# Kernel tuning notes

Measured on AMD Instinct MI355X. Metric: run time of the kernel, lower is better.

The kernel has to match this reference:

```python
import jax, jax.numpy as jnp
import numpy as np

B, D = 65536, 1024

def setup_inputs() -> dict:
    key = jax.random.key(0)
    x = jax.random.normal(key, (B, D), dtype=jnp.float32)
    return {"x": x}

def reference(x) -> jnp.ndarray:
    d = x.shape[1]
    # suffix_norm[:, i] = ||x[:, i:]|| via reverse cumulative sum of squares (single O(D) pass)
    suffix_norm = jnp.sqrt(jnp.cumsum((x * x)[:, ::-1], axis=1)[:, ::-1])
    r = suffix_norm[:, :1]                                   # [B, 1] full norm
    phi = jnp.arccos(x[:, : d - 1] / suffix_norm[:, : d - 1])  # [B, D-1]
    # last angle gets sign correction from the final coordinate
    phi_last = jnp.where(x[:, -1] < 0, 2.0 * jnp.pi - phi[:, -1], phi[:, -1])
    return jnp.concatenate([r, phi[:, : d - 2], phi_last[:, None]], axis=1)
```

## Files before the change

### kernel.cpp

```cpp
#include <hip/hip_runtime.h>
#include <math.h>


#define D_DIM 1024
#define TPB 256

typedef float v4f __attribute__((ext_vector_type(4)));

template <int CTRL>
__device__ __forceinline__ float dpp0(float x) {
    return __builtin_bit_cast(
        float, __builtin_amdgcn_update_dpp(0, __builtin_bit_cast(int, x),
                                           CTRL, 0xF, 0xF, true));
}

__device__ __forceinline__ float rdlane(float x, int l) {
    return __builtin_bit_cast(
        float, __builtin_amdgcn_readlane(__builtin_bit_cast(int, x), l));
}

__device__ __forceinline__ float fast_acos(float x) {
    float a = fabsf(x);
    float p = fmaf(a, -0.0012624911f, 0.0066700901f);
    p = fmaf(p, a, -0.0170881256f);
    p = fmaf(p, a, 0.0308918810f);
    p = fmaf(p, a, -0.0501743046f);
    p = fmaf(p, a, 0.0889789874f);
    p = fmaf(p, a, -0.2145988016f);
    p = fmaf(p, a, 1.5707963050f);
    float r = sqrtf(1.0f - a) * p;
    return x < 0.0f ? 3.14159274101257f - r : r;
}

__device__ __forceinline__ float ang(float num, float den) {
    float r = num * rsqrtf(den);
    r = fminf(1.0f, fmaxf(-1.0f, r));
    return fast_acos(r);
}

__global__ __launch_bounds__(TPB) void tohypersphere_kernel(
    const float* __restrict__ x, float* __restrict__ out) {
    const int t = threadIdx.x;
    const int lane = t & 63;
    const int wave = t >> 6;
    const int r16 = lane >> 4;
    const size_t row_off = (size_t)blockIdx.x * D_DIM;

    const float4 v = ((const float4*)(x + row_off))[t];

    const float s3 = v.w * v.w;
    const float s2 = fmaf(v.z, v.z, s3);
    const float s1 = fmaf(v.y, v.y, s2);
    const float s0 = fmaf(v.x, v.x, s1);

    float ts = s0;
    ts += dpp0<0x101>(ts);
    ts += dpp0<0x102>(ts);
    ts += dpp0<0x104>(ts);
    ts += dpp0<0x108>(ts);

    const float R0 = rdlane(ts, 0);
    const float R1 = rdlane(ts, 16);
    const float R2 = rdlane(ts, 32);
    const float R3 = rdlane(ts, 48);

    float after_rows = 0.0f;
    if (r16 < 1) after_rows += R1;
    if (r16 < 2) after_rows += R2;
    if (r16 < 3) after_rows += R3;
    const float incl_wave = ts + after_rows;
    const float wtot = (R0 + R1) + (R2 + R3);

    __shared__ float wave_tot[4];
    __shared__ float edge_xw[4];
    if (lane == 0) wave_tot[wave] = wtot;
    if (lane == 63) edge_xw[wave] = v.w;

    float xw_prev = __shfl_up(v.w, 1, 64);

    __syncthreads();

    float after_waves = 0.0f;
#pragma unroll
    for (int w = 1; w < 4; ++w)
        if (w > wave) after_waves += wave_tot[w];
    if (lane == 0 && wave > 0) xw_prev = edge_xw[wave - 1];

    const float incl = incl_wave + after_waves;
    const float excl = incl - s0;

    float o0, o1, o2, o3;
    o1 = ang(v.x, incl);
    o2 = ang(v.y, s1 + excl);
    o3 = ang(v.z, s2 + excl);
    if (t == 0) {
        o0 = sqrtf(incl);
    } else {
        o0 = ang(xw_prev, fmaf(xw_prev, xw_prev, incl));
    }
    if (t == TPB - 1 && v.w < 0.0f) {
        o3 = 6.283185307179586476f - o3;
    }

    v4f tv = {o0, o1, o2, o3};
    ((v4f*)(out + row_off))[t] = tv;
}

extern "C" void kernel_launch(void* const* d_in, const int* in_sizes, int n_in,
                              void* d_out, int out_size, void* d_ws, size_t ws_size,
                              hipStream_t stream) {
    const float* x = (const float*)d_in[0];
    float* out = (float*)d_out;
    const int B = in_sizes[0] / D_DIM;
    tohypersphere_kernel<<<B, TPB, 0, stream>>>(x, out);
}
```

Before: 411.9 us.

## Use persistent grid-stride blocks with next-row prefetch and double-buffered scratch

Replaces one-block-per-row launch with a fixed grid of persistent blocks that loop over rows with a grid stride. The next row is loaded before the current row is processed, and the shared-memory scratch is double-buffered so a single barrier per row suffices. This aims to cut block launch overhead and hide load latency, at the cost of fewer independent blocks to supply memory-level parallelism.

```diff
diff --git a/kernel.cpp b/kernel.cpp
--- a/kernel.cpp
+++ b/kernel.cpp
@@ -4,6 +4,7 @@
 
 #define D_DIM 1024
 #define TPB 256
+#define NBLK 2048
 
 typedef float v4f __attribute__((ext_vector_type(4)));
 
@@ -39,71 +40,94 @@
 }
 
 __global__ __launch_bounds__(TPB) void tohypersphere_kernel(
-    const float* __restrict__ x, float* __restrict__ out) {
+    const float* __restrict__ x, float* __restrict__ out, int n_rows) {
     const int t = threadIdx.x;
     const int lane = t & 63;
     const int wave = t >> 6;
     const int r16 = lane >> 4;
-    const size_t row_off = (size_t)blockIdx.x * D_DIM;
 
-    const float4 v = ((const float4*)(x + row_off))[t];
+    __shared__ float wave_tot[2][4];
+    __shared__ float edge_xw[2][4];
 
-    const float s3 = v.w * v.w;
-    const float s2 = fmaf(v.z, v.z, s3);
-    const float s1 = fmaf(v.y, v.y, s2);
-    const float s0 = fmaf(v.x, v.x, s1);
+    const int stride = gridDim.x;
+    int row = blockIdx.x;
+    if (row >= n_rows) return;
 
-    float ts = s0;
-    ts += dpp0<0x101>(ts);
-    ts += dpp0<0x102>(ts);
-    ts += dpp0<0x104>(ts);
-    ts += dpp0<0x108>(ts);
+    const float4* __restrict__ xp = (const float4*)x + t;
+    v4f* __restrict__ op = (v4f*)out + t;
 
-    const float R0 = rdlane(ts, 0);
-    const float R1 = rdlane(ts, 16);
-    const float R2 = rdlane(ts, 32);
-    const float R3 = rdlane(ts, 48);
+    float4 vc = xp[(size_t)row * (D_DIM / 4)];
 
-    float after_rows = 0.0f;
-    if (r16 < 1) after_rows += R1;
-    if (r16 < 2) after_rows += R2;
-    if (r16 < 3) after_rows += R3;
-    const float incl_wave = ts + after_rows;
-    const float wtot = (R0 + R1) + (R2 + R3);
+    int p = 0;
+    while (true) {
+        const int nrow = row + stride;
+        const bool more = (nrow < n_rows);
+        float4 vn;
+        if (more) vn = xp[(size_t)nrow * (D_DIM / 4)];
 
-    __shared__ float wave_tot[4];
-    __shared__ float edge_xw[4];
-    if (lane == 0) wave_tot[wave] = wtot;
-    if (lane == 63) edge_xw[wave] = v.w;
+        const float4 v = vc;
+        const float s3v = v.w * v.w;
+        const float s2v = fmaf(v.z, v.z, s3v);
+        const float s1v = fmaf(v.y, v.y, s2v);
+        const float s0v = fmaf(v.x, v.x, s1v);
 
-    float xw_prev = __shfl_up(v.w, 1, 64);
+        float ts = s0v;
+        ts += dpp0<0x101>(ts);
+        ts += dpp0<0x102>(ts);
+        ts += dpp0<0x104>(ts);
+        ts += dpp0<0x108>(ts);
 
-    __syncthreads();
+        const float R0 = rdlane(ts, 0);
+        const float R1 = rdlane(ts, 16);
+        const float R2 = rdlane(ts, 32);
+        const float R3 = rdlane(ts, 48);
 
-    float after_waves = 0.0f;
+        float after_rows = 0.0f;
+        if (r16 < 1) after_rows += R1;
+        if (r16 < 2) after_rows += R2;
+        if (r16 < 3) after_rows += R3;
+        const float incl_wave = ts + after_rows;
+        const float wtot = (R0 + R1) + (R2 + R3);
+
+        if (lane == 0) wave_tot[p][wave] = wtot;
+        if (lane == 63) edge_xw[p][wave] = v.w;
+
+        float xw_prev = __shfl_up(v.w, 1, 64);
+
+        asm volatile("s_waitcnt lgkmcnt(0)" ::: "memory");
+        __builtin_amdgcn_s_barrier();
+        __builtin_amdgcn_sched_barrier(0);
+
+        float after_waves = 0.0f;
 #pragma unroll
-    for (int w = 1; w < 4; ++w)
-        if (w > wave) after_waves += wave_tot[w];
-    if (lane == 0 && wave > 0) xw_prev = edge_xw[wave - 1];
+        for (int w = 1; w < 4; ++w)
+            if (w > wave) after_waves += wave_tot[p][w];
+        if (lane == 0 && wave > 0) xw_prev = edge_xw[p][wave - 1];
 
-    const float incl = incl_wave + after_waves;
-    const float excl = incl - s0;
+        const float incl = incl_wave + after_waves;
+        const float excl = incl - s0v;
 
-    float o0, o1, o2, o3;
-    o1 = ang(v.x, incl);
-    o2 = ang(v.y, s1 + excl);
-    o3 = ang(v.z, s2 + excl);
-    if (t == 0) {
-        o0 = sqrtf(incl);
-    } else {
-        o0 = ang(xw_prev, fmaf(xw_prev, xw_prev, incl));
+        float o0, o1, o2, o3;
+        o1 = ang(v.x, incl);
+        o2 = ang(v.y, s1v + excl);
+        o3 = ang(v.z, s2v + excl);
+        if (t == 0) {
+            o0 = sqrtf(incl);
+        } else {
+            o0 = ang(xw_prev, fmaf(xw_prev, xw_prev, incl));
+        }
+        if (t == TPB - 1 && v.w < 0.0f) {
+            o3 = 6.283185307179586476f - o3;
+        }
+
+        v4f tv = {o0, o1, o2, o3};
+        op[(size_t)row * (D_DIM / 4)] = tv;
+
+        if (!more) break;
+        row = nrow;
+        vc = vn;
+        p ^= 1;
     }
-    if (t == TPB - 1 && v.w < 0.0f) {
-        o3 = 6.283185307179586476f - o3;
-    }
-
-    v4f tv = {o0, o1, o2, o3};
-    ((v4f*)(out + row_off))[t] = tv;
 }
 
 extern "C" void kernel_launch(void* const* d_in, const int* in_sizes, int n_in,
@@ -112,5 +136,6 @@
     const float* x = (const float*)d_in[0];
     float* out = (float*)d_out;
     const int B = in_sizes[0] / D_DIM;
-    tohypersphere_kernel<<<B, TPB, 0, stream>>>(x, out);
+    const int grid = (B < NBLK) ? B : NBLK;
+    tohypersphere_kernel<<<grid, TPB, 0, stream>>>(x, out, B);
 }
```

New measurement: 434.2 us. 5.4% more time.
